# Kernel tuning notes

Measured on AMD Instinct MI355X. Metric: run time of the kernel, lower is better.

## Reference

```python
import jax, jax.numpy as jnp
import numpy as np

N_HEADS = 16
HEAD_DIM = 64
D_MODEL = N_HEADS * HEAD_DIM  # 1024


def setup_inputs() -> dict:
    key = jax.random.key(0)
    ks = jax.random.split(key, 6)
    B, S, D = 2, 2048, D_MODEL
    s = 0.02
    return {
        "hidden_states": jax.random.normal(ks[0], (B, S, D), jnp.float32),
        "position_bias": jax.random.normal(ks[1], (1, N_HEADS, S, S), jnp.float32),
        "Wq": jax.random.normal(ks[2], (D, D), jnp.float32) * s,
        "Wk": jax.random.normal(ks[3], (D, D), jnp.float32) * s,
        "Wv": jax.random.normal(ks[4], (D, D), jnp.float32) * s,
        "Wo": jax.random.normal(ks[5], (D, D), jnp.float32) * s,
    }


def reference(hidden_states, position_bias, Wq, Wk, Wv, Wo):
    B, S, D = hidden_states.shape

    def split_heads(x):  # [B,S,D] -> [B,H,S,hd]
        return x.reshape(B, S, N_HEADS, HEAD_DIM).transpose(0, 2, 1, 3)

    q = split_heads(hidden_states @ Wq)
    k = split_heads(hidden_states @ Wk)
    v = split_heads(hidden_states @ Wv)

    # T5 attention: NO 1/sqrt(d) scaling; additive relative-position bias.
    scores = jnp.einsum("bhqd,bhkd->bhqk", q, k) + position_bias
    attn = jax.nn.softmax(scores.astype(jnp.float32), axis=-1).astype(scores.dtype)
    ctx = jnp.einsum("bhqk,bhkd->bhqd", attn, v)
    ctx = ctx.transpose(0, 2, 1, 3).reshape(B, S, D)
    return ctx @ Wo
```

## Files before the change

kernel.cpp:

```cpp
#include <hip/hip_runtime.h>
#include <hip/hip_bf16.h>
#include <stdint.h>

typedef __bf16 bf16_t;
typedef __bf16 bf16x8 __attribute__((ext_vector_type(8)));
typedef float  f32x4  __attribute__((ext_vector_type(4)));

#define S_LEN 2048
#define NH    16
#define HD    64
#define DM    1024
#define BATCH 2
#define M_TOT (BATCH * S_LEN)
#define SM_SHIFT 18.0f

__device__ __forceinline__ void gload16(const void* g, void* l) {
    __builtin_amdgcn_global_load_lds(
        (const __attribute__((address_space(1))) unsigned int*)g,
        (__attribute__((address_space(3))) unsigned int*)l, 16, 0, 0);
}

__global__ void convert_h(const float* __restrict__ X, bf16_t* __restrict__ Y, int n) {
    int i = (blockIdx.x * 256 + threadIdx.x) * 4;
    if (i >= n) return;
    float4 v = *(const float4*)(X + i);
    union { bf16_t h[4]; uint2 u; } pk;
    pk.h[0] = (bf16_t)v.x; pk.h[1] = (bf16_t)v.y;
    pk.h[2] = (bf16_t)v.z; pk.h[3] = (bf16_t)v.w;
    *(uint2*)(Y + i) = pk.u;
}

__global__ void convert_transpose_w(const float* __restrict__ W, bf16_t* __restrict__ Wt) {
    __shared__ float tile[32][33];
    const int tid = threadIdx.x;
    const int tx = tid & 31, ty = tid >> 5;
    const int bx = blockIdx.x * 32, by = blockIdx.y * 32;
#pragma unroll
    for (int it = 0; it < 4; ++it)
        tile[ty + it * 8][tx] = W[(size_t)(by + ty + it * 8) * DM + bx + tx];
    __syncthreads();
#pragma unroll
    for (int it = 0; it < 4; ++it)
        Wt[(size_t)(bx + ty + it * 8) * DM + by + tx] = (bf16_t)tile[tx][ty + it * 8];
}

template<int BN, int EPI>
__global__ __launch_bounds__(256)
void gemm_glds(const bf16_t* __restrict__ A, const bf16_t* __restrict__ Bt,
               float* __restrict__ Cf, bf16_t* __restrict__ Qb, bf16_t* __restrict__ Kb,
               bf16_t* __restrict__ Vtb, int M, int N, int K)
{
    constexpr int WN = BN / 2;
    constexpr int NJ = WN / 16;
    constexpr int RB = BN / 32;
    __shared__ bf16_t smem[16640];
    bf16_t* At  = smem;
    bf16_t* Bts = smem + 8192;

    const int tid  = threadIdx.x;
    const int lane = tid & 63;
    const int wave = tid >> 6;
    const int lc = lane & 15;
    const int l4 = lane >> 4;
    const int wr = wave >> 1, wc = wave & 1;
    const int m0 = blockIdx.y * 128;
    const int n0 = blockIdx.x * BN;
    const int srow = tid >> 3;
    const int scol = (tid & 7) * 8;

    f32x4 acc[4][NJ] = {};

    for (int k0 = 0; k0 < K; k0 += 64) {
        __syncthreads();
#pragma unroll
        for (int ro = 0; ro < 4; ++ro)
            gload16(A + (size_t)(m0 + ro * 32 + srow) * K + k0 + scol,
                    At + ro * 2048 + wave * 512);
#pragma unroll
        for (int ro = 0; ro < RB; ++ro)
            gload16(Bt + (size_t)(n0 + ro * 32 + srow) * K + k0 + scol,
                    Bts + ro * 2048 + wave * 512);
        __syncthreads();

        bf16x8 af[2][4], bfr[2][NJ];
#pragma unroll
        for (int kk = 0; kk < 2; ++kk) {
#pragma unroll
            for (int i = 0; i < 4; ++i)
                af[kk][i] = *(const bf16x8*)(At + (wr * 64 + i * 16 + lc) * 64 + kk * 32 + l4 * 8);
#pragma unroll
            for (int j = 0; j < NJ; ++j)
                bfr[kk][j] = *(const bf16x8*)(Bts + (wc * WN + j * 16 + lc) * 64 + kk * 32 + l4 * 8);
        }
#pragma unroll
        for (int kk = 0; kk < 2; ++kk)
#pragma unroll
            for (int i = 0; i < 4; ++i)
#pragma unroll
                for (int j = 0; j < NJ; ++j)
                    acc[i][j] = __builtin_amdgcn_mfma_f32_16x16x32_bf16(af[kk][i], bfr[kk][j], acc[i][j], 0, 0, 0);
    }

    if (EPI == 1) {
#pragma unroll
        for (int i = 0; i < 4; ++i)
#pragma unroll
            for (int j = 0; j < NJ; ++j)
#pragma unroll
                for (int r = 0; r < 4; ++r) {
                    int m = m0 + wr * 64 + i * 16 + l4 * 4 + r;
                    int n = n0 + wc * WN + j * 16 + lc;
                    Cf[(size_t)m * N + n] = acc[i][j][r];
                }
    } else {
        const int sel = n0 >> 10;
        if (sel < 2) {
            bf16_t* Dst = sel == 0 ? Qb : Kb;
#pragma unroll
            for (int i = 0; i < 4; ++i)
#pragma unroll
                for (int j = 0; j < NJ; ++j)
#pragma unroll
                    for (int r = 0; r < 4; ++r) {
                        int m = m0 + wr * 64 + i * 16 + l4 * 4 + r;
                        int n = (n0 & 1023) + wc * WN + j * 16 + lc;
                        int b = m >> 11, s = m & 2047, h = n >> 6, d = n & 63;
                        Dst[(((size_t)(b * NH + h)) * S_LEN + s) * HD + d] = (bf16_t)acc[i][j][r];
                    }
        } else {
            __syncthreads();
            bf16_t* Ct = smem;
#pragma unroll
            for (int i = 0; i < 4; ++i)
#pragma unroll
                for (int j = 0; j < NJ; ++j)
#pragma unroll
                    for (int r = 0; r < 4; ++r) {
                        int ml = wr * 64 + i * 16 + l4 * 4 + r;
                        int nl = wc * WN + j * 16 + lc;
                        Ct[nl * 130 + ml] = (bf16_t)acc[i][j][r];
                    }
            __syncthreads();
            const int rr = tid >> 1, c0 = (tid & 1) * 64;
            const int nn = (n0 - 2048) + rr;
            const int hh = nn >> 6, dd = nn & 63;
            const int bb = m0 >> 11, s0 = m0 & 2047;
            bf16_t* dst = Vtb + (((size_t)(bb * NH + hh)) * HD + dd) * S_LEN + s0 + c0;
            const bf16_t* srcr = Ct + rr * 130 + c0;
#pragma unroll
            for (int u = 0; u < 8; ++u)
                *(uint4*)(dst + u * 8) = *(const uint4*)(srcr + u * 8);
        }
    }
}

__global__ __launch_bounds__(512, 2)
void attn_kernel(const bf16_t* __restrict__ Q, const bf16_t* __restrict__ Kin,
                 const bf16_t* __restrict__ Vt, const float* __restrict__ bias,
                 bf16_t* __restrict__ Ctx)
{
    const int tid  = threadIdx.x;
    const int lane = tid & 63;
    const int wave = tid >> 6;
    const int b    = wave >> 2;
    const int w    = wave & 3;
    const int lc = lane & 15;
    const int l4 = lane >> 4;

    const int f   = blockIdx.x;
    const int xcd = f & 7;
    const int kk_ = f >> 3;
    const int h   = xcd * 2 + (kk_ >> 4);
    const int qt  = kk_ & 15;
    const int qw  = qt * 128 + w * 32;

    __shared__ bf16_t Kt[2][2][64 * 64];
    __shared__ bf16_t Vs[2][2][64 * 64];
    __shared__ bf16_t Pt[8][32 * 68];

    const int bh = b * NH + h;
    const bf16_t* Qg = Q   + (size_t)bh * S_LEN * HD;
    const bf16_t* Kg[2]; const bf16_t* Vg[2];
#pragma unroll
    for (int bb = 0; bb < 2; ++bb) {
        Kg[bb] = Kin + (size_t)(bb * NH + h) * S_LEN * HD;
        Vg[bb] = Vt  + (size_t)(bb * NH + h) * HD * S_LEN;
    }
    const float* Bg = bias + (size_t)h * S_LEN * S_LEN;

    bf16x8 qf[2][2];
#pragma unroll
    for (int i = 0; i < 2; ++i)
#pragma unroll
        for (int kk = 0; kk < 2; ++kk)
            qf[i][kk] = *(const bf16x8*)(Qg + (size_t)(qw + i * 16 + lc) * HD + kk * 32 + l4 * 8);

    f32x4 cacc[2][4] = {};
    float lsum[2][4] = {};

    const int r0   = lane >> 3;
    const int gsrc = (lane & 7) ^ r0;
    const int sb   = wave >> 2;
    const int z    = wave & 3;

    auto stage = [&](int t, int pbuf) {
        const int kv0 = t * 64;
#pragma unroll
        for (int c = 0; c < 2; ++c) {
            const int R = (c * 4 + z) * 8;
            gload16(Kg[sb] + (size_t)(kv0 + R + r0) * HD + gsrc * 8, &Kt[sb][pbuf][R * 64]);
            gload16(Vg[sb] + (size_t)(R + r0) * S_LEN + kv0 + gsrc * 8, &Vs[sb][pbuf][R * 64]);
        }
    };

    auto loadbias = [&](int t, float (&bv)[2][4][4]) {
        const int kv0 = t * 64;
#pragma unroll
        for (int i = 0; i < 2; ++i)
#pragma unroll
            for (int r = 0; r < 4; ++r) {
                const float* bp = Bg + (size_t)(qw + i * 16 + l4 * 4 + r) * S_LEN + kv0 + lc;
#pragma unroll
                for (int j = 0; j < 4; ++j)
                    bv[i][j][r] = bp[j * 16] - SM_SHIFT;
            }
    };

    bf16_t* Pw = Pt[wave];

    auto round = [&](int t, float (&bcur)[2][4][4], float (&bnext)[2][4][4]) {
        const int buf = t & 1;
        if (t < 31) {
            stage(t + 1, buf ^ 1);
            loadbias(t + 1, bnext);
        }
        f32x4 sa[2][4] = {};
        __builtin_amdgcn_s_setprio(1);
#pragma unroll
        for (int kk = 0; kk < 2; ++kk) {
            bf16x8 kf[4];
#pragma unroll
            for (int j = 0; j < 4; ++j)
                kf[j] = *(const bf16x8*)(&Kt[b][buf][(j * 16 + lc) * 64 + (((kk * 4 + l4) ^ (lc & 7)) * 8)]);
#pragma unroll
            for (int i = 0; i < 2; ++i)
#pragma unroll
                for (int j = 0; j < 4; ++j)
                    sa[i][j] = __builtin_amdgcn_mfma_f32_16x16x32_bf16(qf[i][kk], kf[j], sa[i][j], 0, 0, 0);
        }
        __builtin_amdgcn_s_setprio(0);
#pragma unroll
        for (int i = 0; i < 2; ++i)
#pragma unroll
            for (int r = 0; r < 4; ++r) {
                float p0 = __expf(sa[i][0][r] + bcur[i][0][r]);
                float p1 = __expf(sa[i][1][r] + bcur[i][1][r]);
                float p2 = __expf(sa[i][2][r] + bcur[i][2][r]);
                float p3 = __expf(sa[i][3][r] + bcur[i][3][r]);
                lsum[i][r] += (p0 + p1) + (p2 + p3);
                const int rowo = (i * 16 + l4 * 4 + r) * 68 + lc;
                Pw[rowo]      = (bf16_t)p0;
                Pw[rowo + 16] = (bf16_t)p1;
                Pw[rowo + 32] = (bf16_t)p2;
                Pw[rowo + 48] = (bf16_t)p3;
            }
        __builtin_amdgcn_s_setprio(1);
#pragma unroll
        for (int ks = 0; ks < 2; ++ks) {
            bf16x8 pf[2], vf[4];
#pragma unroll
            for (int i = 0; i < 2; ++i)
                pf[i] = *(const bf16x8*)(&Pw[(i * 16 + lc) * 68 + ks * 32 + l4 * 8]);
#pragma unroll
            for (int jd = 0; jd < 4; ++jd)
                vf[jd] = *(const bf16x8*)(&Vs[b][buf][(jd * 16 + lc) * 64 + (((ks * 4 + l4) ^ (lc & 7)) * 8)]);
#pragma unroll
            for (int i = 0; i < 2; ++i)
#pragma unroll
                for (int jd = 0; jd < 4; ++jd)
                    cacc[i][jd] = __builtin_amdgcn_mfma_f32_16x16x32_bf16(pf[i], vf[jd], cacc[i][jd], 0, 0, 0);
        }
        __builtin_amdgcn_s_setprio(0);
        __syncthreads();
    };

    float bvA[2][4][4], bvB[2][4][4];
    stage(0, 0);
    loadbias(0, bvA);
    __syncthreads();

    for (int ot = 0; ot < 16; ++ot) {
        round(2 * ot,     bvA, bvB);
        round(2 * ot + 1, bvB, bvA);
    }

#pragma unroll
    for (int d = 1; d < 16; d <<= 1)
#pragma unroll
        for (int i = 0; i < 2; ++i)
#pragma unroll
            for (int r = 0; r < 4; ++r)
                lsum[i][r] += __shfl_xor(lsum[i][r], d, 64);

    bf16_t* Co = Ctx + (size_t)b * S_LEN * DM + (size_t)h * HD;
#pragma unroll
    for (int i = 0; i < 2; ++i)
#pragma unroll
        for (int r = 0; r < 4; ++r) {
            float rinv = 1.0f / lsum[i][r];
            int qrow = qw + i * 16 + l4 * 4 + r;
#pragma unroll
            for (int jd = 0; jd < 4; ++jd)
                Co[(size_t)qrow * DM + jd * 16 + lc] = (bf16_t)(cacc[i][jd][r] * rinv);
        }
}

extern "C" void kernel_launch(void* const* d_in, const int* in_sizes, int n_in,
                              void* d_out, int out_size, void* d_ws, size_t ws_size,
                              hipStream_t stream)
{
    (void)in_sizes; (void)n_in; (void)out_size; (void)ws_size;
    const float* hs   = (const float*)d_in[0];
    const float* bias = (const float*)d_in[1];
    const float* Wq   = (const float*)d_in[2];
    const float* Wk   = (const float*)d_in[3];
    const float* Wv   = (const float*)d_in[4];
    const float* Wo   = (const float*)d_in[5];
    float* out = (float*)d_out;

    char* ws = (char*)d_ws;
    bf16_t* Hbf   = (bf16_t*)(ws);
    bf16_t* Wqkvt = (bf16_t*)(ws + ( 8u << 20));
    bf16_t* Wot   = (bf16_t*)(ws + (14u << 20));
    bf16_t* Qb    = (bf16_t*)(ws + (16u << 20));
    bf16_t* Kb    = (bf16_t*)(ws + (24u << 20));
    bf16_t* Vtb   = (bf16_t*)(ws + (32u << 20));
    bf16_t* Ctx   = (bf16_t*)(ws + (40u << 20));

    convert_h<<<4096, 256, 0, stream>>>(hs, Hbf, M_TOT * DM);
    dim3 tg(32, 32);
    convert_transpose_w<<<tg, 256, 0, stream>>>(Wq, Wqkvt);
    convert_transpose_w<<<tg, 256, 0, stream>>>(Wk, Wqkvt + (size_t)DM * DM);
    convert_transpose_w<<<tg, 256, 0, stream>>>(Wv, Wqkvt + (size_t)2 * DM * DM);
    convert_transpose_w<<<tg, 256, 0, stream>>>(Wo, Wot);

    dim3 gq(3 * DM / 128, M_TOT / 128);
    gemm_glds<128, 0><<<gq, 256, 0, stream>>>(Hbf, Wqkvt, nullptr, Qb, Kb, Vtb,
                                              M_TOT, 3 * DM, DM);

    attn_kernel<<<256, 512, 0, stream>>>(Qb, Kb, Vtb, bias, Ctx);

    dim3 go(DM / 64, M_TOT / 128);
    gemm_glds<64, 1><<<go, 256, 0, stream>>>(Ctx, Wot, out, nullptr, nullptr, nullptr,
                                             M_TOT, DM, DM);
}
```

Before: 210.3 us.

## Load K/V fragments directly from global into registers, drop LDS staging and barriers

The attention kernel stops staging K and V tiles into shared memory with async global-to-LDS loads. Each wave now loads its own K and V MFMA fragments straight from global memory into registers, prefetching the next tile after the current one is consumed, and the per-round __syncthreads is removed. Before, the two batch groups of waves in a block shared the staging work; now each wave issues its own global loads and relies on L2 reuse, which adds global traffic and register pressure. The four weight convert-transpose launches are also merged into one launch using a z grid dimension.

Result: slower. 304.5 us (+44.8%).

```diff
diff --git a/kernel.cpp b/kernel.cpp
--- a/kernel.cpp
+++ b/kernel.cpp
@@ -30,8 +30,13 @@
     *(uint2*)(Y + i) = pk.u;
 }
 
-__global__ void convert_transpose_w(const float* __restrict__ W, bf16_t* __restrict__ Wt) {
+__global__ void convert_transpose_w4(const float* __restrict__ W0, const float* __restrict__ W1,
+                                     const float* __restrict__ W2, const float* __restrict__ W3,
+                                     bf16_t* __restrict__ D0, bf16_t* __restrict__ D3) {
     __shared__ float tile[32][33];
+    const int z = blockIdx.z;
+    const float* W = z == 0 ? W0 : z == 1 ? W1 : z == 2 ? W2 : W3;
+    bf16_t* Wt = z < 3 ? D0 + (size_t)z * DM * DM : D3;
     const int tid = threadIdx.x;
     const int tx = tid & 31, ty = tid >> 5;
     const int bx = blockIdx.x * 32, by = blockIdx.y * 32;
@@ -174,19 +179,14 @@
     const int qt  = kk_ & 15;
     const int qw  = qt * 128 + w * 32;
 
-    __shared__ bf16_t Kt[2][2][64 * 64];
-    __shared__ bf16_t Vs[2][2][64 * 64];
     __shared__ bf16_t Pt[8][32 * 68];
+    bf16_t* Pw = Pt[wave];
 
     const int bh = b * NH + h;
     const bf16_t* Qg = Q   + (size_t)bh * S_LEN * HD;
-    const bf16_t* Kg[2]; const bf16_t* Vg[2];
-#pragma unroll
-    for (int bb = 0; bb < 2; ++bb) {
-        Kg[bb] = Kin + (size_t)(bb * NH + h) * S_LEN * HD;
-        Vg[bb] = Vt  + (size_t)(bb * NH + h) * HD * S_LEN;
-    }
-    const float* Bg = bias + (size_t)h * S_LEN * S_LEN;
+    const bf16_t* Kg = Kin + (size_t)bh * S_LEN * HD;
+    const bf16_t* Vg = Vt  + (size_t)bh * HD * S_LEN;
+    const float*  Bg = bias + (size_t)h * S_LEN * S_LEN;
 
     bf16x8 qf[2][2];
 #pragma unroll
@@ -198,21 +198,23 @@
     f32x4 cacc[2][4] = {};
     float lsum[2][4] = {};
 
-    const int r0   = lane >> 3;
-    const int gsrc = (lane & 7) ^ r0;
-    const int sb   = wave >> 2;
-    const int z    = wave & 3;
-
-    auto stage = [&](int t, int pbuf) {
-        const int kv0 = t * 64;
-#pragma unroll
-        for (int c = 0; c < 2; ++c) {
-            const int R = (c * 4 + z) * 8;
-            gload16(Kg[sb] + (size_t)(kv0 + R + r0) * HD + gsrc * 8, &Kt[sb][pbuf][R * 64]);
-            gload16(Vg[sb] + (size_t)(R + r0) * S_LEN + kv0 + gsrc * 8, &Vs[sb][pbuf][R * 64]);
-        }
+    bf16x8 kf[2][4];
+    bf16x8 vf[2][4];
+
+    auto loadK = [&](int kv0) {
+#pragma unroll
+        for (int kk = 0; kk < 2; ++kk)
+#pragma unroll
+            for (int j = 0; j < 4; ++j)
+                kf[kk][j] = *(const bf16x8*)(Kg + (size_t)(kv0 + j * 16 + lc) * HD + kk * 32 + l4 * 8);
     };
-
+    auto loadV = [&](int kv0) {
+#pragma unroll
+        for (int ks = 0; ks < 2; ++ks)
+#pragma unroll
+            for (int jd = 0; jd < 4; ++jd)
+                vf[ks][jd] = *(const bf16x8*)(Vg + (size_t)(jd * 16 + lc) * S_LEN + kv0 + ks * 32 + l4 * 8);
+    };
     auto loadbias = [&](int t, float (&bv)[2][4][4]) {
         const int kv0 = t * 64;
 #pragma unroll
@@ -226,29 +228,23 @@
             }
     };
 
-    bf16_t* Pw = Pt[wave];
-
     auto round = [&](int t, float (&bcur)[2][4][4], float (&bnext)[2][4][4]) {
-        const int buf = t & 1;
-        if (t < 31) {
-            stage(t + 1, buf ^ 1);
-            loadbias(t + 1, bnext);
-        }
+        const int kvn = (t + 1) * 64;
+        if (t < 31) loadbias(t + 1, bnext);
+
         f32x4 sa[2][4] = {};
         __builtin_amdgcn_s_setprio(1);
 #pragma unroll
-        for (int kk = 0; kk < 2; ++kk) {
-            bf16x8 kf[4];
-#pragma unroll
-            for (int j = 0; j < 4; ++j)
-                kf[j] = *(const bf16x8*)(&Kt[b][buf][(j * 16 + lc) * 64 + (((kk * 4 + l4) ^ (lc & 7)) * 8)]);
+        for (int kk = 0; kk < 2; ++kk)
 #pragma unroll
             for (int i = 0; i < 2; ++i)
 #pragma unroll
                 for (int j = 0; j < 4; ++j)
-                    sa[i][j] = __builtin_amdgcn_mfma_f32_16x16x32_bf16(qf[i][kk], kf[j], sa[i][j], 0, 0, 0);
-        }
+                    sa[i][j] = __builtin_amdgcn_mfma_f32_16x16x32_bf16(qf[i][kk], kf[kk][j], sa[i][j], 0, 0, 0);
         __builtin_amdgcn_s_setprio(0);
+
+        if (t < 31) loadK(kvn);
+
 #pragma unroll
         for (int i = 0; i < 2; ++i)
 #pragma unroll
@@ -264,30 +260,29 @@
                 Pw[rowo + 32] = (bf16_t)p2;
                 Pw[rowo + 48] = (bf16_t)p3;
             }
+
         __builtin_amdgcn_s_setprio(1);
 #pragma unroll
         for (int ks = 0; ks < 2; ++ks) {
-            bf16x8 pf[2], vf[4];
+            bf16x8 pf[2];
 #pragma unroll
             for (int i = 0; i < 2; ++i)
                 pf[i] = *(const bf16x8*)(&Pw[(i * 16 + lc) * 68 + ks * 32 + l4 * 8]);
 #pragma unroll
-            for (int jd = 0; jd < 4; ++jd)
-                vf[jd] = *(const bf16x8*)(&Vs[b][buf][(jd * 16 + lc) * 64 + (((ks * 4 + l4) ^ (lc & 7)) * 8)]);
-#pragma unroll
             for (int i = 0; i < 2; ++i)
 #pragma unroll
                 for (int jd = 0; jd < 4; ++jd)
-                    cacc[i][jd] = __builtin_amdgcn_mfma_f32_16x16x32_bf16(pf[i], vf[jd], cacc[i][jd], 0, 0, 0);
+                    cacc[i][jd] = __builtin_amdgcn_mfma_f32_16x16x32_bf16(pf[i], vf[ks][jd], cacc[i][jd], 0, 0, 0);
         }
         __builtin_amdgcn_s_setprio(0);
-        __syncthreads();
+
+        if (t < 31) loadV(kvn);
     };
 
     float bvA[2][4][4], bvB[2][4][4];
-    stage(0, 0);
+    loadK(0);
+    loadV(0);
     loadbias(0, bvA);
-    __syncthreads();
 
     for (int ot = 0; ot < 16; ++ot) {
         round(2 * ot,     bvA, bvB);
@@ -338,11 +333,8 @@
     bf16_t* Ctx   = (bf16_t*)(ws + (40u << 20));
 
     convert_h<<<4096, 256, 0, stream>>>(hs, Hbf, M_TOT * DM);
-    dim3 tg(32, 32);
-    convert_transpose_w<<<tg, 256, 0, stream>>>(Wq, Wqkvt);
-    convert_transpose_w<<<tg, 256, 0, stream>>>(Wk, Wqkvt + (size_t)DM * DM);
-    convert_transpose_w<<<tg, 256, 0, stream>>>(Wv, Wqkvt + (size_t)2 * DM * DM);
-    convert_transpose_w<<<tg, 256, 0, stream>>>(Wo, Wot);
+    dim3 tg(32, 32, 4);
+    convert_transpose_w4<<<tg, 256, 0, stream>>>(Wq, Wk, Wv, Wo, Wqkvt, Wot);
 
     dim3 gq(3 * DM / 128, M_TOT / 128);
     gemm_glds<128, 0><<<gq, 256, 0, stream>>>(Hbf, Wqkvt, nullptr, Qb, Kb, Vtb,
```

## Transpose QK MFMA so bias loads vectorize and merge weight conversions

Applied to the files above, without the earlier changes.

The score MFMA operands are swapped so each lane holds four consecutive key columns for one query row. That lets the position-bias loads become 16-byte vector loads and the P writes to LDS become packed bf16x4 stores. The row-sum reduction now runs across the 4 lane groups and is redistributed with shuffles. The four weight transpose-convert launches are merged into one 3D grid, the K/V staging is simplified to one row slice per wave, and launch bounds are relaxed to one block per SIMD, which may change register allocation and occupancy.

Measured after the change: 220.3 us. 4.8% more time.

```diff
diff --git a/kernel.cpp b/kernel.cpp
--- a/kernel.cpp
+++ b/kernel.cpp
@@ -3,6 +3,7 @@
 #include <stdint.h>
 
 typedef __bf16 bf16_t;
+typedef __bf16 bf16x4 __attribute__((ext_vector_type(4)));
 typedef __bf16 bf16x8 __attribute__((ext_vector_type(8)));
 typedef float  f32x4  __attribute__((ext_vector_type(4)));
 
@@ -30,8 +31,13 @@
     *(uint2*)(Y + i) = pk.u;
 }
 
-__global__ void convert_transpose_w(const float* __restrict__ W, bf16_t* __restrict__ Wt) {
+__global__ void convert_transpose_w4(const float* __restrict__ W0, const float* __restrict__ W1,
+                                     const float* __restrict__ W2, const float* __restrict__ W3,
+                                     bf16_t* __restrict__ D0, bf16_t* __restrict__ D3) {
     __shared__ float tile[32][33];
+    const int z = blockIdx.z;
+    const float* W = z == 0 ? W0 : z == 1 ? W1 : z == 2 ? W2 : W3;
+    bf16_t* Wt = z < 3 ? D0 + (size_t)z * DM * DM : D3;
     const int tid = threadIdx.x;
     const int tx = tid & 31, ty = tid >> 5;
     const int bx = blockIdx.x * 32, by = blockIdx.y * 32;
@@ -154,7 +160,7 @@
     }
 }
 
-__global__ __launch_bounds__(512, 2)
+__global__ __launch_bounds__(512, 1)
 void attn_kernel(const bf16_t* __restrict__ Q, const bf16_t* __restrict__ Kin,
                  const bf16_t* __restrict__ Vt, const float* __restrict__ bias,
                  bf16_t* __restrict__ Ctx)
@@ -177,9 +183,9 @@
     __shared__ bf16_t Kt[2][2][64 * 64];
     __shared__ bf16_t Vs[2][2][64 * 64];
     __shared__ bf16_t Pt[8][32 * 68];
-
-    const int bh = b * NH + h;
-    const bf16_t* Qg = Q   + (size_t)bh * S_LEN * HD;
+    bf16_t* Pw = Pt[wave];
+
+    const bf16_t* Qg = Q + (size_t)(b * NH + h) * S_LEN * HD;
     const bf16_t* Kg[2]; const bf16_t* Vg[2];
 #pragma unroll
     for (int bb = 0; bb < 2; ++bb) {
@@ -196,45 +202,40 @@
             qf[i][kk] = *(const bf16x8*)(Qg + (size_t)(qw + i * 16 + lc) * HD + kk * 32 + l4 * 8);
 
     f32x4 cacc[2][4] = {};
-    float lsum[2][4] = {};
+    float lsum[2] = {};
 
     const int r0   = lane >> 3;
     const int gsrc = (lane & 7) ^ r0;
-    const int sb   = wave >> 2;
-    const int z    = wave & 3;
+    const int R    = wave * 8;
 
     auto stage = [&](int t, int pbuf) {
         const int kv0 = t * 64;
-#pragma unroll
-        for (int c = 0; c < 2; ++c) {
-            const int R = (c * 4 + z) * 8;
-            gload16(Kg[sb] + (size_t)(kv0 + R + r0) * HD + gsrc * 8, &Kt[sb][pbuf][R * 64]);
-            gload16(Vg[sb] + (size_t)(R + r0) * S_LEN + kv0 + gsrc * 8, &Vs[sb][pbuf][R * 64]);
-        }
+        gload16(Kg[0] + (size_t)(kv0 + R + r0) * HD + gsrc * 8, &Kt[0][pbuf][R * 64]);
+        gload16(Kg[1] + (size_t)(kv0 + R + r0) * HD + gsrc * 8, &Kt[1][pbuf][R * 64]);
+        gload16(Vg[0] + (size_t)(R + r0) * S_LEN + kv0 + gsrc * 8, &Vs[0][pbuf][R * 64]);
+        gload16(Vg[1] + (size_t)(R + r0) * S_LEN + kv0 + gsrc * 8, &Vs[1][pbuf][R * 64]);
     };
 
-    auto loadbias = [&](int t, float (&bv)[2][4][4]) {
+    auto loadbias = [&](int t, f32x4 (&bv)[2][4]) {
         const int kv0 = t * 64;
 #pragma unroll
         for (int i = 0; i < 2; ++i)
 #pragma unroll
-            for (int r = 0; r < 4; ++r) {
-                const float* bp = Bg + (size_t)(qw + i * 16 + l4 * 4 + r) * S_LEN + kv0 + lc;
-#pragma unroll
-                for (int j = 0; j < 4; ++j)
-                    bv[i][j][r] = bp[j * 16] - SM_SHIFT;
+            for (int j = 0; j < 4; ++j) {
+                f32x4 v = *(const f32x4*)(Bg + (size_t)(qw + i * 16 + lc) * S_LEN + kv0 + j * 16 + l4 * 4);
+                bv[i][j] = v - SM_SHIFT;
             }
     };
 
-    bf16_t* Pw = Pt[wave];
-
-    auto round = [&](int t, float (&bcur)[2][4][4], float (&bnext)[2][4][4]) {
+    auto round = [&](int t, f32x4 (&bcur)[2][4], f32x4 (&bnext)[2][4]) {
         const int buf = t & 1;
         if (t < 31) {
             stage(t + 1, buf ^ 1);
             loadbias(t + 1, bnext);
         }
-        f32x4 sa[2][4] = {};
+        __builtin_amdgcn_sched_barrier(0);
+
+        f32x4 saT[4][2] = {};
         __builtin_amdgcn_s_setprio(1);
 #pragma unroll
         for (int kk = 0; kk < 2; ++kk) {
@@ -243,27 +244,25 @@
             for (int j = 0; j < 4; ++j)
                 kf[j] = *(const bf16x8*)(&Kt[b][buf][(j * 16 + lc) * 64 + (((kk * 4 + l4) ^ (lc & 7)) * 8)]);
 #pragma unroll
-            for (int i = 0; i < 2; ++i)
-#pragma unroll
-                for (int j = 0; j < 4; ++j)
-                    sa[i][j] = __builtin_amdgcn_mfma_f32_16x16x32_bf16(qf[i][kk], kf[j], sa[i][j], 0, 0, 0);
+            for (int j = 0; j < 4; ++j)
+#pragma unroll
+                for (int i = 0; i < 2; ++i)
+                    saT[j][i] = __builtin_amdgcn_mfma_f32_16x16x32_bf16(kf[j], qf[i][kk], saT[j][i], 0, 0, 0);
         }
         __builtin_amdgcn_s_setprio(0);
-#pragma unroll
-        for (int i = 0; i < 2; ++i)
-#pragma unroll
-            for (int r = 0; r < 4; ++r) {
-                float p0 = __expf(sa[i][0][r] + bcur[i][0][r]);
-                float p1 = __expf(sa[i][1][r] + bcur[i][1][r]);
-                float p2 = __expf(sa[i][2][r] + bcur[i][2][r]);
-                float p3 = __expf(sa[i][3][r] + bcur[i][3][r]);
-                lsum[i][r] += (p0 + p1) + (p2 + p3);
-                const int rowo = (i * 16 + l4 * 4 + r) * 68 + lc;
-                Pw[rowo]      = (bf16_t)p0;
-                Pw[rowo + 16] = (bf16_t)p1;
-                Pw[rowo + 32] = (bf16_t)p2;
-                Pw[rowo + 48] = (bf16_t)p3;
+
+#pragma unroll
+        for (int i = 0; i < 2; ++i) {
+#pragma unroll
+            for (int j = 0; j < 4; ++j) {
+                f32x4 s = saT[j][i] + bcur[i][j];
+                float p0 = __expf(s.x), p1 = __expf(s.y), p2 = __expf(s.z), p3 = __expf(s.w);
+                lsum[i] += (p0 + p1) + (p2 + p3);
+                bf16x4 pk = {(bf16_t)p0, (bf16_t)p1, (bf16_t)p2, (bf16_t)p3};
+                *(bf16x4*)(&Pw[(i * 16 + lc) * 68 + j * 16 + l4 * 4]) = pk;
             }
+        }
+
         __builtin_amdgcn_s_setprio(1);
 #pragma unroll
         for (int ks = 0; ks < 2; ++ks) {
@@ -278,13 +277,16 @@
             for (int i = 0; i < 2; ++i)
 #pragma unroll
                 for (int jd = 0; jd < 4; ++jd)
-                    cacc[i][jd] = __builtin_amdgcn_mfma_f32_16x16x32_bf16(pf[i], vf[jd], cacc[i][jd], 0, 0, 0);
+                    cacc[i][jd] = __builtin_amdgcn_mfma_f32_16x16x32_bf16(pf[i], vf[ks == 0 ? jd : jd], cacc[i][jd], 0, 0, 0),
+                    (void)0;
+#pragma unroll
+            for (int i = 0; i < 2; ++i) (void)pf[i];
         }
         __builtin_amdgcn_s_setprio(0);
         __syncthreads();
     };
 
-    float bvA[2][4][4], bvB[2][4][4];
+    f32x4 bvA[2][4], bvB[2][4];
     stage(0, 0);
     loadbias(0, bvA);
     __syncthreads();
@@ -295,23 +297,26 @@
     }
 
 #pragma unroll
-    for (int d = 1; d < 16; d <<= 1)
-#pragma unroll
-        for (int i = 0; i < 2; ++i)
-#pragma unroll
-            for (int r = 0; r < 4; ++r)
-                lsum[i][r] += __shfl_xor(lsum[i][r], d, 64);
+    for (int i = 0; i < 2; ++i) {
+        lsum[i] += __shfl_xor(lsum[i], 16, 64);
+        lsum[i] += __shfl_xor(lsum[i], 32, 64);
+    }
+    float rinv[2][4];
+#pragma unroll
+    for (int i = 0; i < 2; ++i)
+#pragma unroll
+        for (int r = 0; r < 4; ++r)
+            rinv[i][r] = 1.0f / __shfl(lsum[i], l4 * 4 + r, 16);
 
     bf16_t* Co = Ctx + (size_t)b * S_LEN * DM + (size_t)h * HD;
 #pragma unroll
     for (int i = 0; i < 2; ++i)
 #pragma unroll
         for (int r = 0; r < 4; ++r) {
-            float rinv = 1.0f / lsum[i][r];
             int qrow = qw + i * 16 + l4 * 4 + r;
 #pragma unroll
             for (int jd = 0; jd < 4; ++jd)
-                Co[(size_t)qrow * DM + jd * 16 + lc] = (bf16_t)(cacc[i][jd][r] * rinv);
+                Co[(size_t)qrow * DM + jd * 16 + lc] = (bf16_t)(cacc[i][jd][r] * rinv[i][r]);
         }
 }
 
@@ -338,11 +343,8 @@
     bf16_t* Ctx   = (bf16_t*)(ws + (40u << 20));
 
     convert_h<<<4096, 256, 0, stream>>>(hs, Hbf, M_TOT * DM);
-    dim3 tg(32, 32);
-    convert_transpose_w<<<tg, 256, 0, stream>>>(Wq, Wqkvt);
-    convert_transpose_w<<<tg, 256, 0, stream>>>(Wk, Wqkvt + (size_t)DM * DM);
-    convert_transpose_w<<<tg, 256, 0, stream>>>(Wv, Wqkvt + (size_t)2 * DM * DM);
-    convert_transpose_w<<<tg, 256, 0, stream>>>(Wo, Wot);
+    dim3 tg(32, 32, 4);
+    convert_transpose_w4<<<tg, 256, 0, stream>>>(Wq, Wk, Wv, Wo, Wqkvt, Wot);
 
     dim3 gq(3 * DM / 128, M_TOT / 128);
     gemm_glds<128, 0><<<gq, 256, 0, stream>>>(Hbf, Wqkvt, nullptr, Qb, Kb, Vtb,
```
